# Kernel optimization log

Hardware: AMD Instinct MI355X
Metric: run time of the kernel (lower is better)

The kernel has to match this reference:

```python
import jax, jax.numpy as jnp
import numpy as np

B, S, D = 2, 2048, 1024
E, K, F = 8, 2, 4 * 1024  # num_experts, top_k, fc_rate*embed_dim
T = B * S


def setup_inputs() -> dict:
    key = jax.random.key(0)
    ks = jax.random.split(key, 8)
    w = lambda k, shape: jax.random.normal(k, shape, jnp.float32) * 0.02
    return {
        "hidden_states": jax.random.normal(ks[0], (B, S, D), jnp.float32),
        "noise": jax.random.normal(ks[1], (T, E), jnp.float32),  # randn_like in router
        "Wg": w(ks[2], (D, E)), "bg": jnp.zeros((E,), jnp.float32),
        "Wn": w(ks[3], (D, E)), "bn": jnp.zeros((E,), jnp.float32),
        "W1": w(ks[4], (E, D, F)), "b1": jnp.zeros((E, F), jnp.float32),
        "W2": w(ks[5], (E, F, D)), "b2": jnp.zeros((E, D), jnp.float32),
    }


def reference(hidden_states, noise, Wg, bg, Wn, bn, W1, b1, W2, b2):
    b, s, d = hidden_states.shape
    x = hidden_states.reshape(-1, d)  # [T, D]

    # --- NoisyTopkRouter ---
    gate_logits = x @ Wg + bg                        # [T, E]
    noise_logits = x @ Wn + bn                       # [T, E]
    noisy_logits = gate_logits + noise * jax.nn.softplus(noise_logits)
    rw = jax.nn.softmax(noisy_logits.astype(jnp.float32), axis=-1)
    top_w, top_i = jax.lax.top_k(rw, K)              # [T, K]
    top_w = top_w / top_w.sum(-1, keepdims=True)
    top_w = top_w.astype(x.dtype)

    # Dense per-token combine coefficients: coef[t,e] = sum_k top_w[t,k]*[top_i[t,k]==e]
    tok = jnp.arange(x.shape[0])[:, None]
    coef = jnp.zeros((x.shape[0], E), x.dtype).at[tok, top_i].add(top_w)  # [T, E]

    # --- Experts: Linear -> GELU(exact) -> Linear (dropout = identity, eval mode) ---
    h = jax.nn.gelu(jnp.einsum('td,edf->tef', x, W1) + b1, approximate=False)  # [T,E,F]
    y = jnp.einsum('tef,efd->ted', h, W2) + b2                                  # [T,E,D]
    out = jnp.einsum('ted,te->td', y, coef)                                     # [T,D]

    return out.reshape(b, s, d), noisy_logits, gate_logits
```

## Files before the change

kernel.cpp:

```cpp
#include <hip/hip_runtime.h>
#include <hip/hip_bf16.h>

#define T_TOK 4096
#define D_DIM 1024
#define E_NUM 8
#define F_DIM 4096
#define NPAIR 8192

#define BM 256
#define BN 256
#define BK 32

typedef float f32x4 __attribute__((ext_vector_type(4)));
typedef __bf16 bf16x8 __attribute__((ext_vector_type(8)));
typedef unsigned short u16x8 __attribute__((ext_vector_type(8)));
typedef unsigned short u16x4 __attribute__((ext_vector_type(4)));

__device__ __forceinline__ unsigned short f2bf(float f) {
    unsigned int u = __float_as_uint(f);
    u += 0x7fffu + ((u >> 16) & 1u);
    return (unsigned short)(u >> 16);
}

typedef const __attribute__((address_space(1))) void GV;
typedef __attribute__((address_space(3))) void LV;

__device__ __forceinline__ void load_lds16(const void* g, void* l) {
    __builtin_amdgcn_global_load_lds((GV*)g, (LV*)l, 16, 0, 0);
}

__device__ __forceinline__ int swz4(int r) { return (r ^ (r >> 2)) & 3; }

__device__ __forceinline__ bf16x8 lds_frag32(const unsigned short* S, int row, int cb) {
    int byte = row * 64 + ((cb ^ swz4(row)) << 4);
    return *(const bf16x8*)((const char*)S + byte);
}

__global__ __launch_bounds__(256) void router_convert_kernel(
    const float* __restrict__ x, const float* __restrict__ noise,
    const float* __restrict__ Wg, const float* __restrict__ bg,
    const float* __restrict__ Wn, const float* __restrict__ bn,
    float* __restrict__ out_noisy, float* __restrict__ out_gate,
    int* __restrict__ tk_idx, float* __restrict__ tk_w,
    unsigned short* __restrict__ xb)
{
    int lane = threadIdx.x & 63;
    int t = blockIdx.x * 4 + (threadIdx.x >> 6);
    const float* xr = x + (size_t)t * D_DIM;
    unsigned short* xbr = xb + (size_t)t * D_DIM;

    #pragma unroll
    for (int r = 0; r < 4; ++r) {
        int d = r * 256 + lane * 4;
        float4 v = *(const float4*)(xr + d);
        u16x4 o;
        o[0] = f2bf(v.x); o[1] = f2bf(v.y); o[2] = f2bf(v.z); o[3] = f2bf(v.w);
        *(u16x4*)(xbr + d) = o;
    }

    float ag[E_NUM] = {}, an[E_NUM] = {};
    for (int it = 0; it < D_DIM / 64; ++it) {
        int d = it * 64 + lane;
        float xv = xr[d];
        float4 g0 = *(const float4*)(Wg + (size_t)d * E_NUM);
        float4 g1 = *(const float4*)(Wg + (size_t)d * E_NUM + 4);
        float4 m0 = *(const float4*)(Wn + (size_t)d * E_NUM);
        float4 m1 = *(const float4*)(Wn + (size_t)d * E_NUM + 4);
        ag[0] += xv * g0.x; ag[1] += xv * g0.y; ag[2] += xv * g0.z; ag[3] += xv * g0.w;
        ag[4] += xv * g1.x; ag[5] += xv * g1.y; ag[6] += xv * g1.z; ag[7] += xv * g1.w;
        an[0] += xv * m0.x; an[1] += xv * m0.y; an[2] += xv * m0.z; an[3] += xv * m0.w;
        an[4] += xv * m1.x; an[5] += xv * m1.y; an[6] += xv * m1.z; an[7] += xv * m1.w;
    }
    #pragma unroll
    for (int off = 32; off > 0; off >>= 1) {
        #pragma unroll
        for (int e = 0; e < E_NUM; ++e) {
            ag[e] += __shfl_xor(ag[e], off);
            an[e] += __shfl_xor(an[e], off);
        }
    }
    if (lane == 0) {
        float nz[E_NUM];
        #pragma unroll
        for (int e = 0; e < E_NUM; ++e) {
            float g = ag[e] + bg[e];
            float nn = an[e] + bn[e];
            float sp = fmaxf(nn, 0.f) + log1pf(expf(-fabsf(nn)));
            float z = g + noise[(size_t)t * E_NUM + e] * sp;
            out_gate[(size_t)t * E_NUM + e] = g;
            out_noisy[(size_t)t * E_NUM + e] = z;
            nz[e] = z;
        }
        int e0 = 0;
        #pragma unroll
        for (int e = 1; e < E_NUM; ++e) if (nz[e] > nz[e0]) e0 = e;
        int e1 = (e0 == 0) ? 1 : 0;
        #pragma unroll
        for (int e = 0; e < E_NUM; ++e) if (e != e0 && nz[e] > nz[e1]) e1 = e;
        float b = expf(nz[e1] - nz[e0]);
        float w0 = 1.f / (1.f + b);
        float w1 = b / (1.f + b);
        tk_idx[t * 2] = e0;  tk_idx[t * 2 + 1] = e1;
        tk_w[t * 2] = w0;    tk_w[t * 2 + 1] = w1;
    }
}

__global__ __launch_bounds__(256) void scan_scatter_kernel(
    const int* __restrict__ tk_idx,
    int* __restrict__ perm, int* __restrict__ meta)
{
    __shared__ int cnt[256][E_NUM];
    __shared__ int soff[E_NUM];
    int tid = threadIdx.x;
    const int PPT = NPAIR / 256;
    int p0 = tid * PPT;

    int c[E_NUM] = {};
    for (int i = 0; i < PPT; ++i) c[tk_idx[p0 + i]]++;
    #pragma unroll
    for (int e = 0; e < E_NUM; ++e) cnt[tid][e] = c[e];
    __syncthreads();

    if (tid < E_NUM) {
        int s = 0;
        for (int j = 0; j < 256; ++j) { int v = cnt[j][tid]; cnt[j][tid] = s; s += v; }
        soff[tid] = s;
    }
    __syncthreads();

    if (tid == 0) {
        int off = 0, nt = 0;
        for (int e = 0; e < E_NUM; ++e) {
            int ce = soff[e];
            meta[1 + e] = off;
            meta[9 + e] = ce;
            for (int j = 0; j < ce; j += BM) {
                meta[32 + nt]  = e;
                meta[160 + nt] = off + j;
                meta[288 + nt] = off + ce;
                nt++;
            }
            off += ce;
        }
        meta[0] = nt;
    }
    __syncthreads();
    if (tid < E_NUM) soff[tid] = meta[1 + tid];
    __syncthreads();

    int pos[E_NUM];
    #pragma unroll
    for (int e = 0; e < E_NUM; ++e) pos[e] = soff[e] + cnt[tid][e];
    for (int i = 0; i < PPT; ++i) {
        int e = tk_idx[p0 + i];
        perm[pos[e]++] = p0 + i;
    }
}

__global__ __launch_bounds__(256) void transpose_kernel(
    const float* __restrict__ W, unsigned short* __restrict__ WT, int R, int C)
{
    __shared__ float tile[64][65];
    int e = blockIdx.z;
    int c0 = blockIdx.x * 64, r0 = blockIdx.y * 64;
    int tx = threadIdx.x & 15, ty = threadIdx.x >> 4;
    const float* src = W + (size_t)e * R * C;
    #pragma unroll
    for (int j = 0; j < 4; ++j) {
        int r = ty + 16 * j;
        float4 v = *(const float4*)(src + (size_t)(r0 + r) * C + c0 + tx * 4);
        *(float4*)&tile[r][tx * 4] = v;
    }
    __syncthreads();
    unsigned short* dst = WT + (size_t)e * C * R;
    int sx = threadIdx.x & 7, sy = threadIdx.x >> 3;
    #pragma unroll
    for (int j = 0; j < 2; ++j) {
        int c = sy + 32 * j;
        u16x8 o;
        #pragma unroll
        for (int k = 0; k < 8; ++k) o[k] = f2bf(tile[sx * 8 + k][c]);
        *(u16x8*)(dst + (size_t)(c0 + c) * R + r0 + sx * 8) = o;
    }
}

#define GEMM_COMPUTE(Abuf, Bbuf) do {                                                      \
    bf16x8 af[4], bf[4];                                                                   \
    _Pragma("unroll")                                                                      \
    for (int m_ = 0; m_ < 4; ++m_)                                                         \
        af[m_] = lds_frag32((Abuf), wm + m_ * 16 + (lane & 15), lane >> 4);                \
    _Pragma("unroll")                                                                      \
    for (int n_ = 0; n_ < 4; ++n_)                                                         \
        bf[n_] = lds_frag32((Bbuf), wn + n_ * 16 + (lane & 15), lane >> 4);                \
    _Pragma("unroll")                                                                      \
    for (int m_ = 0; m_ < 4; ++m_)                                                         \
        _Pragma("unroll")                                                                  \
        for (int n_ = 0; n_ < 4; ++n_)                                                     \
            acc[m_][n_] = __builtin_amdgcn_mfma_f32_16x16x32_bf16(af[m_], bf[n_],          \
                                                                  acc[m_][n_], 0, 0, 0);  \
} while (0)

#define GEMM_LOOP(NT, STAGE) do {                                                          \
    STAGE(0, 0);                                                                           \
    for (int t = 0; t < (NT); ++t) {                                                       \
        int cbuf = t & 1;                                                                  \
        if (t + 1 < (NT)) {                                                                \
            STAGE((t + 1) * BK, cbuf ^ 1);                                                 \
            asm volatile("s_waitcnt vmcnt(2)" ::: "memory");                               \
        } else {                                                                           \
            asm volatile("s_waitcnt vmcnt(0)" ::: "memory");                               \
        }                                                                                  \
        __builtin_amdgcn_s_barrier();                                                      \
        __builtin_amdgcn_s_setprio(1);                                                     \
        GEMM_COMPUTE(As[cbuf], Bs[cbuf]);                                                  \
        __builtin_amdgcn_s_setprio(0);                                                     \
        asm volatile("s_waitcnt lgkmcnt(0)" ::: "memory");                                 \
        __builtin_amdgcn_s_barrier();                                                      \
    }                                                                                      \
} while (0)

__global__ __launch_bounds__(1024, 4) void fc1_kernel(
    const unsigned short* __restrict__ xb,
    const unsigned short* __restrict__ W1T,
    const float* __restrict__ b1,
    const int* __restrict__ perm,
    const int* __restrict__ meta,
    unsigned short* __restrict__ h)
{
    __shared__ __align__(16) unsigned short As[2][BM * BK];
    __shared__ __align__(16) unsigned short Bs[2][BN * BK];

    int nt = meta[0];
    int total = nt * 16;
    int ipx = (total + 7) >> 3;
    int xcd = blockIdx.x & 7;
    int slot = blockIdx.x >> 3;
    int lim = (xcd + 1) * ipx; if (lim > total) lim = total;

    int tid = threadIdx.x, lane = tid & 63, wv = tid >> 6;
    int wm = (wv >> 2) * 64, wn = (wv & 3) * 64;
    int row_st = wv * 16 + (lane >> 2);
    int slot_st = lane & 3;
    int csw = ((slot_st ^ swz4(row_st)) * 8);
    unsigned short* ldsA = &As[0][0] + wv * 512 + lane * 8;
    unsigned short* ldsB = &Bs[0][0] + wv * 512 + lane * 8;

    for (int item = xcd * ipx + slot; item < lim; item += 32) {
        int tile = item >> 4;
        int n0 = (item & 15) * BN;
        int e    = meta[32 + tile];
        int rs   = meta[160 + tile];
        int rend = meta[288 + tile];

        int pos = rs + row_st; if (pos >= NPAIR) pos = NPAIR - 1;
        const unsigned short* aptr = xb + (size_t)(perm[pos] >> 1) * D_DIM + csw;
        const unsigned short* bptr = W1T + ((size_t)e * F_DIM + n0 + row_st) * D_DIM + csw;

        f32x4 acc[4][4] = {};

#define STAGE1(k0, b) do {                                         \
    load_lds16(aptr + (k0), ldsA + (b) * (BM * BK));               \
    load_lds16(bptr + (k0), ldsB + (b) * (BN * BK));               \
} while (0)

        GEMM_LOOP(D_DIM / BK, STAGE1);
#undef STAGE1

        #pragma unroll
        for (int m = 0; m < 4; ++m) {
            #pragma unroll
            for (int j = 0; j < 4; ++j) {
                int r = wm + m * 16 + (lane >> 4) * 4 + j;
                int p = rs + r;
                if (p >= rend) continue;
                #pragma unroll
                for (int n = 0; n < 4; ++n) {
                    int col = n0 + wn + n * 16 + (lane & 15);
                    float v = acc[m][n][j] + b1[e * F_DIM + col];
                    v = 0.5f * v * (1.f + erff(v * 0.70710678118654752f));
                    h[(size_t)p * F_DIM + col] = f2bf(v);
                }
            }
        }
        __builtin_amdgcn_s_barrier();
    }
}

__global__ __launch_bounds__(1024, 4) void fc2_kernel(
    const unsigned short* __restrict__ h,
    const unsigned short* __restrict__ W2T,
    const float* __restrict__ b2,
    const int* __restrict__ perm,
    const float* __restrict__ tk_w,
    const int* __restrict__ meta,
    float* __restrict__ out)
{
    __shared__ __align__(16) unsigned short As[2][BM * BK];
    __shared__ __align__(16) unsigned short Bs[2][BN * BK];

    int nt = meta[0];
    int total = nt * 8;
    int ipx = (total + 7) >> 3;
    int xcd = blockIdx.x & 7;
    int slot = blockIdx.x >> 3;
    int lim = (xcd + 1) * ipx; if (lim > total) lim = total;

    int tid = threadIdx.x, lane = tid & 63, wv = tid >> 6;
    int wm = (wv >> 2) * 64, wn = (wv & 3) * 64;
    int row_st = wv * 16 + (lane >> 2);
    int slot_st = lane & 3;
    int csw = ((slot_st ^ swz4(row_st)) * 8);
    unsigned short* ldsA = &As[0][0] + wv * 512 + lane * 8;
    unsigned short* ldsB = &Bs[0][0] + wv * 512 + lane * 8;

    for (int item = xcd * ipx + slot; item < lim; item += 32) {
        int tile = item >> 3;
        int rem  = item & 7;
        int n0 = (rem >> 1) * BN;
        int ks = rem & 1;
        int kbeg = ks * (F_DIM / 2);
        int e    = meta[32 + tile];
        int rs   = meta[160 + tile];
        int rend = meta[288 + tile];

        int pos = rs + row_st; if (pos >= NPAIR) pos = NPAIR - 1;
        const unsigned short* aptr = h + (size_t)pos * F_DIM + kbeg + csw;
        const unsigned short* bptr = W2T + ((size_t)e * D_DIM + n0 + row_st) * F_DIM + kbeg + csw;

        f32x4 acc[4][4] = {};

#define STAGE2(k0, b) do {                                         \
    load_lds16(aptr + (k0), ldsA + (b) * (BM * BK));               \
    load_lds16(bptr + (k0), ldsB + (b) * (BN * BK));               \
} while (0)

        GEMM_LOOP((F_DIM / 2) / BK, STAGE2);
#undef STAGE2

        #pragma unroll
        for (int m = 0; m < 4; ++m) {
            #pragma unroll
            for (int j = 0; j < 4; ++j) {
                int r = wm + m * 16 + (lane >> 4) * 4 + j;
                int p = rs + r;
                if (p >= rend) continue;
                int pr = perm[p];
                int t2 = pr >> 1;
                float w = tk_w[pr];
                #pragma unroll
                for (int n = 0; n < 4; ++n) {
                    int col = n0 + wn + n * 16 + (lane & 15);
                    float base = (ks == 0) ? b2[e * D_DIM + col] : 0.f;
                    float v = (acc[m][n][j] + base) * w;
                    atomicAdd(&out[(size_t)t2 * D_DIM + col], v);
                }
            }
        }
        __builtin_amdgcn_s_barrier();
    }
}

extern "C" void kernel_launch(void* const* d_in, const int* in_sizes, int n_in,
                              void* d_out, int out_size, void* d_ws, size_t ws_size,
                              hipStream_t stream)
{
    const float* x     = (const float*)d_in[0];
    const float* noise = (const float*)d_in[1];
    const float* Wg    = (const float*)d_in[2];
    const float* bg    = (const float*)d_in[3];
    const float* Wn    = (const float*)d_in[4];
    const float* bn    = (const float*)d_in[5];
    const float* W1    = (const float*)d_in[6];
    const float* b1    = (const float*)d_in[7];
    const float* W2    = (const float*)d_in[8];
    const float* b2    = (const float*)d_in[9];

    float* out       = (float*)d_out;
    float* out_noisy = out + (size_t)T_TOK * D_DIM;
    float* out_gate  = out_noisy + (size_t)T_TOK * E_NUM;

    char* ws = (char*)d_ws;
    int*   tk_idx = (int*)ws;
    float* tk_w   = (float*)(ws + 32768);
    int*   perm   = (int*)(ws + 65536);
    int*   meta   = (int*)(ws + 98304);
    size_t off = 131072;
    unsigned short* xb   = (unsigned short*)(ws + off); off += (size_t)T_TOK * D_DIM * 2;
    unsigned short* W1T  = (unsigned short*)(ws + off); off += (size_t)E_NUM * F_DIM * D_DIM * 2;
    unsigned short* W2T  = (unsigned short*)(ws + off); off += (size_t)E_NUM * D_DIM * F_DIM * 2;
    unsigned short* hbuf = (unsigned short*)(ws + off); off += (size_t)NPAIR * F_DIM * 2;

    hipMemsetAsync(d_out, 0, (size_t)out_size * sizeof(float), stream);

    router_convert_kernel<<<T_TOK / 4, 256, 0, stream>>>(x, noise, Wg, bg, Wn, bn,
                                                         out_noisy, out_gate, tk_idx, tk_w, xb);
    scan_scatter_kernel<<<1, 256, 0, stream>>>(tk_idx, perm, meta);
    transpose_kernel<<<dim3(D_DIM / 64, F_DIM / 64, E_NUM), 256, 0, stream>>>(W2, W2T, F_DIM, D_DIM);
    transpose_kernel<<<dim3(F_DIM / 64, D_DIM / 64, E_NUM), 256, 0, stream>>>(W1, W1T, D_DIM, F_DIM);

    fc1_kernel<<<256, 1024, 0, stream>>>(xb, W1T, b1, perm, meta, hbuf);
    fc2_kernel<<<256, 1024, 0, stream>>>(hbuf, W2T, b2, perm, tk_w, meta, out);
}
```

Baseline: 480.5 us.

## Replace persistent 1024-thread GEMMs with per-wave private-LDS 128x128 tile blocks

Swaps the persistent 256x256-tile, 16-wave cooperative GEMM loops in fc1 and fc2 for non-persistent 256-thread blocks that each compute a 128x128 output tile. Every wave stages and consumes its own 64x64 LDS slice, so no block-wide barriers are needed. The grid is sized for a worst-case tile count (NTMAX) and surplus blocks exit early, with XCD-aware block-to-tile mapping. The intent is to remove barrier stalls and raise occupancy. In exchange, each wave's loads are serialized behind its own compute, there is no cross-wave operand reuse in LDS, and more blocks are launched and immediately discarded.

Measured after the change: 549.3 us. +14.3%, slower.

```diff
diff --git a/kernel.cpp b/kernel.cpp
--- a/kernel.cpp
+++ b/kernel.cpp
@@ -7,9 +7,7 @@
 #define F_DIM 4096
 #define NPAIR 8192
 
-#define BM 256
-#define BN 256
-#define BK 32
+#define NTMAX 39
 
 typedef float f32x4 __attribute__((ext_vector_type(4)));
 typedef __bf16 bf16x8 __attribute__((ext_vector_type(8)));
@@ -29,12 +27,7 @@
     __builtin_amdgcn_global_load_lds((GV*)g, (LV*)l, 16, 0, 0);
 }
 
-__device__ __forceinline__ int swz4(int r) { return (r ^ (r >> 2)) & 3; }
-
-__device__ __forceinline__ bf16x8 lds_frag32(const unsigned short* S, int row, int cb) {
-    int byte = row * 64 + ((cb ^ swz4(row)) << 4);
-    return *(const bf16x8*)((const char*)S + byte);
-}
+__device__ __forceinline__ int fsw(int r) { return ((r >> 1) ^ (r >> 3)) & 3; }
 
 __global__ __launch_bounds__(256) void router_convert_kernel(
     const float* __restrict__ x, const float* __restrict__ noise,
@@ -134,7 +127,7 @@
             int ce = soff[e];
             meta[1 + e] = off;
             meta[9 + e] = ce;
-            for (int j = 0; j < ce; j += BM) {
+            for (int j = 0; j < ce; j += 256) {
                 meta[32 + nt]  = e;
                 meta[160 + nt] = off + j;
                 meta[288 + nt] = off + ce;
@@ -184,42 +177,42 @@
     }
 }
 
-#define GEMM_COMPUTE(Abuf, Bbuf) do {                                                      \
-    bf16x8 af[4], bf[4];                                                                   \
-    _Pragma("unroll")                                                                      \
-    for (int m_ = 0; m_ < 4; ++m_)                                                         \
-        af[m_] = lds_frag32((Abuf), wm + m_ * 16 + (lane & 15), lane >> 4);                \
-    _Pragma("unroll")                                                                      \
-    for (int n_ = 0; n_ < 4; ++n_)                                                         \
-        bf[n_] = lds_frag32((Bbuf), wn + n_ * 16 + (lane & 15), lane >> 4);                \
-    _Pragma("unroll")                                                                      \
-    for (int m_ = 0; m_ < 4; ++m_)                                                         \
-        _Pragma("unroll")                                                                  \
-        for (int n_ = 0; n_ < 4; ++n_)                                                     \
-            acc[m_][n_] = __builtin_amdgcn_mfma_f32_16x16x32_bf16(af[m_], bf[n_],          \
-                                                                  acc[m_][n_], 0, 0, 0);  \
-} while (0)
-
-#define GEMM_LOOP(NT, STAGE) do {                                                          \
-    STAGE(0, 0);                                                                           \
-    for (int t = 0; t < (NT); ++t) {                                                       \
-        int cbuf = t & 1;                                                                  \
-        if (t + 1 < (NT)) {                                                                \
-            STAGE((t + 1) * BK, cbuf ^ 1);                                                 \
-            asm volatile("s_waitcnt vmcnt(2)" ::: "memory");                               \
-        } else {                                                                           \
-            asm volatile("s_waitcnt vmcnt(0)" ::: "memory");                               \
-        }                                                                                  \
-        __builtin_amdgcn_s_barrier();                                                      \
-        __builtin_amdgcn_s_setprio(1);                                                     \
-        GEMM_COMPUTE(As[cbuf], Bs[cbuf]);                                                  \
-        __builtin_amdgcn_s_setprio(0);                                                     \
-        asm volatile("s_waitcnt lgkmcnt(0)" ::: "memory");                                 \
-        __builtin_amdgcn_s_barrier();                                                      \
-    }                                                                                      \
-} while (0)
-
-__global__ __launch_bounds__(1024, 4) void fc1_kernel(
+#define WAVE_GEMM_LOOP(NT)                                                              \
+    for (int t = 0; t < (NT); ++t) {                                                    \
+        asm volatile("s_waitcnt vmcnt(0)" ::: "memory");                                \
+        __builtin_amdgcn_sched_barrier(0);                                              \
+        bf16x8 af[4], bf[4];                                                            \
+        _Pragma("unroll")                                                               \
+        for (int m_ = 0; m_ < 4; ++m_) {                                                \
+            int r_ = m_ * 16 + l15;                                                     \
+            af[m_] = *(const bf16x8*)((const char*)la + r_ * 64 + ((l16 ^ fsw(r_)) << 4)); \
+        }                                                                               \
+        _Pragma("unroll")                                                               \
+        for (int n_ = 0; n_ < 4; ++n_) {                                                \
+            int r_ = n_ * 16 + l15;                                                     \
+            bf[n_] = *(const bf16x8*)((const char*)lb + r_ * 64 + ((l16 ^ fsw(r_)) << 4)); \
+        }                                                                               \
+        asm volatile("s_waitcnt lgkmcnt(0)" ::: "memory");                              \
+        __builtin_amdgcn_sched_barrier(0);                                              \
+        if (t + 1 < (NT)) {                                                             \
+            int k0_ = (t + 1) * 32;                                                     \
+            _Pragma("unroll")                                                           \
+            for (int i_ = 0; i_ < 4; ++i_) {                                            \
+                load_lds16(ap[i_] + k0_, la + i_ * 512);                                \
+                load_lds16(bp[i_] + k0_, lb + i_ * 512);                                \
+            }                                                                           \
+        }                                                                               \
+        __builtin_amdgcn_s_setprio(1);                                                  \
+        _Pragma("unroll")                                                               \
+        for (int m_ = 0; m_ < 4; ++m_)                                                  \
+            _Pragma("unroll")                                                           \
+            for (int n_ = 0; n_ < 4; ++n_)                                              \
+                acc[m_][n_] = __builtin_amdgcn_mfma_f32_16x16x32_bf16(af[m_], bf[n_],   \
+                                                                      acc[m_][n_], 0, 0, 0); \
+        __builtin_amdgcn_s_setprio(0);                                                  \
+    }
+
+__global__ __launch_bounds__(256, 4) void fc1_kernel(
     const unsigned short* __restrict__ xb,
     const unsigned short* __restrict__ W1T,
     const float* __restrict__ b1,
@@ -227,66 +220,64 @@
     const int* __restrict__ meta,
     unsigned short* __restrict__ h)
 {
-    __shared__ __align__(16) unsigned short As[2][BM * BK];
-    __shared__ __align__(16) unsigned short Bs[2][BN * BK];
-
     int nt = meta[0];
-    int total = nt * 16;
-    int ipx = (total + 7) >> 3;
-    int xcd = blockIdx.x & 7;
-    int slot = blockIdx.x >> 3;
-    int lim = (xcd + 1) * ipx; if (lim > total) lim = total;
-
-    int tid = threadIdx.x, lane = tid & 63, wv = tid >> 6;
-    int wm = (wv >> 2) * 64, wn = (wv & 3) * 64;
-    int row_st = wv * 16 + (lane >> 2);
-    int slot_st = lane & 3;
-    int csw = ((slot_st ^ swz4(row_st)) * 8);
-    unsigned short* ldsA = &As[0][0] + wv * 512 + lane * 8;
-    unsigned short* ldsB = &Bs[0][0] + wv * 512 + lane * 8;
-
-    for (int item = xcd * ipx + slot; item < lim; item += 32) {
-        int tile = item >> 4;
-        int n0 = (item & 15) * BN;
-        int e    = meta[32 + tile];
-        int rs   = meta[160 + tile];
-        int rend = meta[288 + tile];
-
-        int pos = rs + row_st; if (pos >= NPAIR) pos = NPAIR - 1;
-        const unsigned short* aptr = xb + (size_t)(perm[pos] >> 1) * D_DIM + csw;
-        const unsigned short* bptr = W1T + ((size_t)e * F_DIM + n0 + row_st) * D_DIM + csw;
-
-        f32x4 acc[4][4] = {};
-
-#define STAGE1(k0, b) do {                                         \
-    load_lds16(aptr + (k0), ldsA + (b) * (BM * BK));               \
-    load_lds16(bptr + (k0), ldsB + (b) * (BN * BK));               \
-} while (0)
-
-        GEMM_LOOP(D_DIM / BK, STAGE1);
-#undef STAGE1
-
-        #pragma unroll
-        for (int m = 0; m < 4; ++m) {
+    int bid = blockIdx.x;
+    int xcd = bid & 7;
+    int idx = bid >> 3;
+    int n0i = xcd * 4 + (idx & 3);
+    int mb  = idx >> 2;
+    int tile = mb >> 1, mhalf = mb & 1;
+    if (tile >= nt) return;
+    int e = meta[32 + tile], rs = meta[160 + tile], rend = meta[288 + tile];
+
+    __shared__ __align__(16) unsigned short As[4][2048];
+    __shared__ __align__(16) unsigned short Bs[4][2048];
+
+    int lane = threadIdx.x & 63, wv = threadIdx.x >> 6;
+    int wr = wv >> 1, wc = wv & 1;
+    int l15 = lane & 15, l16 = lane >> 4;
+
+    int rowA = mhalf * 128 + wr * 64;
+    int colB = n0i * 128 + wc * 64;
+
+    const unsigned short* ap[4];
+    const unsigned short* bp[4];
+    #pragma unroll
+    for (int i = 0; i < 4; ++i) {
+        int lr = i * 16 + (lane >> 2);
+        int csw = ((lane & 3) ^ fsw(lr)) * 8;
+        int pos = rs + rowA + lr; if (pos >= NPAIR) pos = NPAIR - 1;
+        ap[i] = xb + (size_t)(perm[pos] >> 1) * D_DIM + csw;
+        bp[i] = W1T + ((size_t)e * F_DIM + colB + lr) * D_DIM + csw;
+    }
+    unsigned short* la = As[wv];
+    unsigned short* lb = Bs[wv];
+
+    f32x4 acc[4][4] = {};
+
+    #pragma unroll
+    for (int i = 0; i < 4; ++i) { load_lds16(ap[i], la + i * 512); load_lds16(bp[i], lb + i * 512); }
+
+    WAVE_GEMM_LOOP(D_DIM / 32)
+
+    #pragma unroll
+    for (int m = 0; m < 4; ++m) {
+        #pragma unroll
+        for (int j = 0; j < 4; ++j) {
+            int p = rs + rowA + m * 16 + l16 * 4 + j;
+            if (p >= rend) continue;
             #pragma unroll
-            for (int j = 0; j < 4; ++j) {
-                int r = wm + m * 16 + (lane >> 4) * 4 + j;
-                int p = rs + r;
-                if (p >= rend) continue;
-                #pragma unroll
-                for (int n = 0; n < 4; ++n) {
-                    int col = n0 + wn + n * 16 + (lane & 15);
-                    float v = acc[m][n][j] + b1[e * F_DIM + col];
-                    v = 0.5f * v * (1.f + erff(v * 0.70710678118654752f));
-                    h[(size_t)p * F_DIM + col] = f2bf(v);
-                }
+            for (int n = 0; n < 4; ++n) {
+                int col = colB + n * 16 + l15;
+                float v = acc[m][n][j] + b1[e * F_DIM + col];
+                v = 0.5f * v * (1.f + erff(v * 0.70710678118654752f));
+                h[(size_t)p * F_DIM + col] = f2bf(v);
             }
         }
-        __builtin_amdgcn_s_barrier();
-    }
-}
-
-__global__ __launch_bounds__(1024, 4) void fc2_kernel(
+    }
+}
+
+__global__ __launch_bounds__(256, 4) void fc2_kernel(
     const unsigned short* __restrict__ h,
     const unsigned short* __restrict__ W2T,
     const float* __restrict__ b2,
@@ -295,68 +286,65 @@
     const int* __restrict__ meta,
     float* __restrict__ out)
 {
-    __shared__ __align__(16) unsigned short As[2][BM * BK];
-    __shared__ __align__(16) unsigned short Bs[2][BN * BK];
-
     int nt = meta[0];
-    int total = nt * 8;
-    int ipx = (total + 7) >> 3;
-    int xcd = blockIdx.x & 7;
-    int slot = blockIdx.x >> 3;
-    int lim = (xcd + 1) * ipx; if (lim > total) lim = total;
-
-    int tid = threadIdx.x, lane = tid & 63, wv = tid >> 6;
-    int wm = (wv >> 2) * 64, wn = (wv & 3) * 64;
-    int row_st = wv * 16 + (lane >> 2);
-    int slot_st = lane & 3;
-    int csw = ((slot_st ^ swz4(row_st)) * 8);
-    unsigned short* ldsA = &As[0][0] + wv * 512 + lane * 8;
-    unsigned short* ldsB = &Bs[0][0] + wv * 512 + lane * 8;
-
-    for (int item = xcd * ipx + slot; item < lim; item += 32) {
-        int tile = item >> 3;
-        int rem  = item & 7;
-        int n0 = (rem >> 1) * BN;
-        int ks = rem & 1;
-        int kbeg = ks * (F_DIM / 2);
-        int e    = meta[32 + tile];
-        int rs   = meta[160 + tile];
-        int rend = meta[288 + tile];
-
-        int pos = rs + row_st; if (pos >= NPAIR) pos = NPAIR - 1;
-        const unsigned short* aptr = h + (size_t)pos * F_DIM + kbeg + csw;
-        const unsigned short* bptr = W2T + ((size_t)e * D_DIM + n0 + row_st) * F_DIM + kbeg + csw;
-
-        f32x4 acc[4][4] = {};
-
-#define STAGE2(k0, b) do {                                         \
-    load_lds16(aptr + (k0), ldsA + (b) * (BM * BK));               \
-    load_lds16(bptr + (k0), ldsB + (b) * (BN * BK));               \
-} while (0)
-
-        GEMM_LOOP((F_DIM / 2) / BK, STAGE2);
-#undef STAGE2
-
-        #pragma unroll
-        for (int m = 0; m < 4; ++m) {
+    int bid = blockIdx.x;
+    int xcd = bid & 7;
+    int idx = bid >> 3;
+    int n0i = xcd;
+    int ks  = idx & 1;
+    int mb  = idx >> 1;
+    int tile = mb >> 1, mhalf = mb & 1;
+    if (tile >= nt) return;
+    int e = meta[32 + tile], rs = meta[160 + tile], rend = meta[288 + tile];
+    int kbeg = ks * (F_DIM / 2);
+
+    __shared__ __align__(16) unsigned short As[4][2048];
+    __shared__ __align__(16) unsigned short Bs[4][2048];
+
+    int lane = threadIdx.x & 63, wv = threadIdx.x >> 6;
+    int wr = wv >> 1, wc = wv & 1;
+    int l15 = lane & 15, l16 = lane >> 4;
+
+    int rowA = mhalf * 128 + wr * 64;
+    int colB = n0i * 128 + wc * 64;
+
+    const unsigned short* ap[4];
+    const unsigned short* bp[4];
+    #pragma unroll
+    for (int i = 0; i < 4; ++i) {
+        int lr = i * 16 + (lane >> 2);
+        int csw = ((lane & 3) ^ fsw(lr)) * 8;
+        int pos = rs + rowA + lr; if (pos >= NPAIR) pos = NPAIR - 1;
+        ap[i] = h + (size_t)pos * F_DIM + kbeg + csw;
+        bp[i] = W2T + ((size_t)e * D_DIM + colB + lr) * F_DIM + kbeg + csw;
+    }
+    unsigned short* la = As[wv];
+    unsigned short* lb = Bs[wv];
+
+    f32x4 acc[4][4] = {};
+
+    #pragma unroll
+    for (int i = 0; i < 4; ++i) { load_lds16(ap[i], la + i * 512); load_lds16(bp[i], lb + i * 512); }
+
+    WAVE_GEMM_LOOP((F_DIM / 2) / 32)
+
+    #pragma unroll
+    for (int m = 0; m < 4; ++m) {
+        #pragma unroll
+        for (int j = 0; j < 4; ++j) {
+            int p = rs + rowA + m * 16 + l16 * 4 + j;
+            if (p >= rend) continue;
+            int pr = perm[p];
+            int t2 = pr >> 1;
+            float w = tk_w[pr];
             #pragma unroll
-            for (int j = 0; j < 4; ++j) {
-                int r = wm + m * 16 + (lane >> 4) * 4 + j;
-                int p = rs + r;
-                if (p >= rend) continue;
-                int pr = perm[p];
-                int t2 = pr >> 1;
-                float w = tk_w[pr];
-                #pragma unroll
-                for (int n = 0; n < 4; ++n) {
-                    int col = n0 + wn + n * 16 + (lane & 15);
-                    float base = (ks == 0) ? b2[e * D_DIM + col] : 0.f;
-                    float v = (acc[m][n][j] + base) * w;
-                    atomicAdd(&out[(size_t)t2 * D_DIM + col], v);
-                }
+            for (int n = 0; n < 4; ++n) {
+                int col = colB + n * 16 + l15;
+                float base = (ks == 0) ? b2[e * D_DIM + col] : 0.f;
+                float v = (acc[m][n][j] + base) * w;
+                atomicAdd(&out[(size_t)t2 * D_DIM + col], v);
             }
         }
-        __builtin_amdgcn_s_barrier();
     }
 }
 
@@ -398,6 +386,6 @@
     transpose_kernel<<<dim3(D_DIM / 64, F_DIM / 64, E_NUM), 256, 0, stream>>>(W2, W2T, F_DIM, D_DIM);
     transpose_kernel<<<dim3(F_DIM / 64, D_DIM / 64, E_NUM), 256, 0, stream>>>(W1, W1T, D_DIM, F_DIM);
 
-    fc1_kernel<<<256, 1024, 0, stream>>>(xb, W1T, b1, perm, meta, hbuf);
-    fc2_kernel<<<256, 1024, 0, stream>>>(hbuf, W2T, b2, perm, tk_w, meta, out);
-}
+    fc1_kernel<<<8 * 4 * (NTMAX * 2), 256, 0, stream>>>(xb, W1T, b1, perm, meta, hbuf);
+    fc2_kernel<<<8 * 2 * (NTMAX * 2), 256, 0, stream>>>(hbuf, W2T, b2, perm, tk_w, meta, out);
+}
```
